# Optimization experiments

Hardware: AMD Instinct MI355X
Metric: run time of the kernel (lower is better)

Reference implementation:

```python
import jax, jax.numpy as jnp
import numpy as np

B, S, DM, TD, H, HD = 2, 2048, 1024, 1024, 16, 64


def setup_inputs() -> dict:
    key = jax.random.key(0)
    k1, k2, k3, k4 = jax.random.split(key, 4)
    query = jax.random.normal(k1, (B, S, DM), dtype=jnp.float32)
    # fused QKV projection weight (nn.Linear weight layout: [out, in]) and output proj
    W_in = jax.random.normal(k2, (3 * TD, DM), dtype=jnp.float32) * 0.02
    W_out = jax.random.normal(k3, (DM, TD), dtype=jnp.float32) * 0.02
    # standard RoPE tables, broadcastable against [B, H, S, HD]
    inv_freq = 1.0 / (10000.0 ** (jnp.arange(0, HD, 2, dtype=jnp.float32) / HD))
    t = jnp.arange(S, dtype=jnp.float32)
    freqs = jnp.outer(t, inv_freq)                      # [S, HD/2]
    emb = jnp.concatenate([freqs, freqs], axis=-1)      # [S, HD]
    sin_q = jnp.sin(emb)[None, None]                    # [1,1,S,HD]
    cos_q = jnp.cos(emb)[None, None]
    # padding mask over keys: first length[b] positions valid (>= S/2 so no NaN rows)
    lengths = jax.random.randint(k4, (B,), S // 2, S + 1)
    attn_mask = jnp.arange(S)[None, :] < lengths[:, None]  # [B, S] bool
    return {"query": query, "W_in": W_in, "W_out": W_out,
            "sin_q": sin_q, "cos_q": cos_q, "attn_mask": attn_mask}


def _rotate_half(x):
    x1, x2 = jnp.split(x, 2, axis=-1)
    return jnp.concatenate([-x2, x1], axis=-1)


def reference(query, W_in, W_out, sin_q, cos_q, attn_mask):
    # fused QKV projection (proj_in, bias=False)
    qkv = query @ W_in.T                                # [B, S, 3*TD]
    q, k, v = jnp.split(qkv, 3, axis=-1)
    to_heads = lambda x: x.reshape(B, S, H, HD).transpose(0, 2, 1, 3)  # [B,H,S,HD]
    q, k, v = to_heads(q), to_heads(k), to_heads(v)
    # RoPE (prefix = 0 since sin covers full sequence)
    q = q * cos_q + _rotate_half(q) * sin_q
    k = k * cos_q + _rotate_half(k) * sin_q
    # SDPA with padding-mask bias + causal mask
    scale = 1.0 / jnp.sqrt(jnp.float32(HD))
    scores = jnp.einsum('bhqd,bhkd->bhqk', q, k) * scale  # [B,H,S,S]
    causal = jnp.arange(S)[:, None] >= jnp.arange(S)[None, :]  # [S, S]
    mask = attn_mask[:, None, None, :] & causal[None, None]    # [B,1,S,S]
    scores = jnp.where(mask, scores, -jnp.inf)
    attn = jax.nn.softmax(scores, axis=-1)
    out = jnp.einsum('bhqk,bhkd->bhqd', attn, v)        # [B,H,S,HD]
    out = out.transpose(0, 2, 1, 3).reshape(B, S, TD)
    return out @ W_out.T                                 # [B, S, DM]
```

## Files before the change

### kernel.cpp

```cpp
#include <hip/hip_runtime.h>
#include <hip/hip_bf16.h>

#define B_ 2
#define S_ 2048
#define DM_ 1024
#define TD_ 1024
#define H_ 16
#define HD_ 64

using bf16 = __hip_bfloat16;
typedef __attribute__((ext_vector_type(8))) short s8v;
typedef __attribute__((ext_vector_type(4))) float f4v;

__device__ __forceinline__ f4v mfma_bf16(s8v a, s8v b, f4v c) {
    return __builtin_amdgcn_mfma_f32_16x16x32_bf16(a, b, c, 0, 0, 0);
}

__device__ __forceinline__ unsigned cvt_pk_bf16(float a, float b) {
    unsigned r;
    asm("v_cvt_pk_bf16_f32 %0, %1, %2" : "=v"(r) : "v"(a), "v"(b));
    return r;
}
__device__ __forceinline__ int2 pack4bf(float a, float b, float c, float d) {
    int2 r;
    r.x = (int)cvt_pk_bf16(a, b);
    r.y = (int)cvt_pk_bf16(c, d);
    return r;
}

__device__ __forceinline__ bool detect_f32(const unsigned int* __restrict__ cosw) {
    return (cosw[0] & 0xFFFFu) == 0u;
}

__device__ __forceinline__ float ld_f(const void* p, int idx, bool f32) {
    return f32 ? ((const float*)p)[idx]
               : __bfloat162float(((const bf16*)p)[idx]);
}

__device__ __forceinline__ void gload_lds16(const bf16* g, void* l) {
    __builtin_amdgcn_global_load_lds(
        (const __attribute__((address_space(1))) unsigned int*)(const void*)g,
        (__attribute__((address_space(3))) unsigned int*)l,
        16, 0, 0);
}

#define NQ_  (B_ * S_ * DM_)
#define NWI_ (3 * TD_ * DM_)
#define NWO_ (DM_ * TD_)
#define NCVT_BLOCKS ((NQ_ + NWI_ + NWO_) / 2048)

__global__ __launch_bounds__(256)
void prep_all(const void* __restrict__ q, const void* __restrict__ wi,
              const void* __restrict__ wo, bf16* __restrict__ dst,
              const void* __restrict__ mask, int* __restrict__ lengths,
              const unsigned int* __restrict__ cosw) {
    const int bid = blockIdx.x;
    if (bid < NCVT_BLOCKS) {
        const bool f32 = detect_f32(cosw);
        int i = (bid * 256 + threadIdx.x) * 8;
        const void* src; int off;
        if (i < NQ_)              { src = q;  off = i; }
        else if (i < NQ_ + NWI_)  { src = wi; off = i - NQ_; }
        else                      { src = wo; off = i - NQ_ - NWI_; }
        if (f32) {
            const float* p = (const float*)src + off;
            float4 x = *reinterpret_cast<const float4*>(p);
            float4 y = *reinterpret_cast<const float4*>(p + 4);
            union { unsigned u[4]; int4 v; } t;
            t.u[0] = cvt_pk_bf16(x.x, x.y);
            t.u[1] = cvt_pk_bf16(x.z, x.w);
            t.u[2] = cvt_pk_bf16(y.x, y.y);
            t.u[3] = cvt_pk_bf16(y.z, y.w);
            *reinterpret_cast<int4*>(dst + i) = t.v;
        } else {
            *reinterpret_cast<int4*>(dst + i) =
                *reinterpret_cast<const int4*>((const bf16*)src + off);
        }
        return;
    }
    int b = bid - NCVT_BLOCKS;
    unsigned int w0 = ((const unsigned int*)mask)[0];
    int enc;
    if (w0 == 1u) enc = 0;
    else if (w0 == 0x01010101u) enc = 1;
    else if (w0 == 0x3F803F80u) enc = 2;
    else enc = 3;
    int cnt = 0;
    for (int s = threadIdx.x; s < S_; s += 256) {
        int i = b * S_ + s;
        bool v;
        if (enc == 0)      v = ((const int*)mask)[i] != 0;
        else if (enc == 1) v = ((const unsigned char*)mask)[i] != 0;
        else if (enc == 2) v = ((const unsigned short*)mask)[i] != 0;
        else               v = ((const float*)mask)[i] != 0.f;
        cnt += v ? 1 : 0;
    }
    __shared__ int red[256];
    red[threadIdx.x] = cnt;
    __syncthreads();
    for (int off = 128; off > 0; off >>= 1) {
        if (threadIdx.x < off) red[threadIdx.x] += red[threadIdx.x + off];
        __syncthreads();
    }
    if (threadIdx.x == 0) lengths[b] = red[0];
}

__global__ __launch_bounds__(256)
void gemm_nt(const bf16* __restrict__ A, const bf16* __restrict__ Bm,
             void* __restrict__ C, int M, int N, int K,
             int c_dyn, const unsigned int* __restrict__ cosw) {
    __shared__ bf16 lds_a[128 * 64];
    __shared__ bf16 lds_b[128 * 64];

    const bool cf32 = c_dyn && detect_f32(cosw);

    const int t = threadIdx.x;
    const int wave = t >> 6, lane = t & 63;
    const int quad = lane >> 4, l16 = lane & 15;
    const int wm = wave >> 1, wn = wave & 1;
    const int m0 = blockIdx.y * 128, n0 = blockIdx.x * 128;
    const int wuni = __builtin_amdgcn_readfirstlane(wave);

    f4v acc[4][4];
    #pragma unroll
    for (int i = 0; i < 4; i++)
        #pragma unroll
        for (int j = 0; j < 4; j++)
            acc[i][j] = f4v{0.f, 0.f, 0.f, 0.f};

    for (int k0 = 0; k0 < K; k0 += 64) {
        __syncthreads();
        #pragma unroll
        for (int i = 0; i < 4; i++) {
            int ci = i * 256 + t;
            int row = ci >> 3;
            int csrc = (ci & 7) ^ (row & 7);
            gload_lds16(A + (size_t)(m0 + row) * K + k0 + csrc * 8,
                        (char*)lds_a + i * 4096 + wuni * 1024);
            gload_lds16(Bm + (size_t)(n0 + row) * K + k0 + csrc * 8,
                        (char*)lds_b + i * 4096 + wuni * 1024);
        }
        __syncthreads();

        #pragma unroll
        for (int kk = 0; kk < 2; kk++) {
            s8v afr[4], bfr[4];
            #pragma unroll
            for (int mb = 0; mb < 4; mb++) {
                int r = wm * 64 + mb * 16 + l16;
                int ch = (kk * 4 + quad) ^ (l16 & 7);
                afr[mb] = *reinterpret_cast<const s8v*>(&lds_a[r * 64 + ch * 8]);
            }
            #pragma unroll
            for (int nb = 0; nb < 4; nb++) {
                int r = wn * 64 + nb * 16 + l16;
                int ch = (kk * 4 + quad) ^ (l16 & 7);
                bfr[nb] = *reinterpret_cast<const s8v*>(&lds_b[r * 64 + ch * 8]);
            }
            #pragma unroll
            for (int mb = 0; mb < 4; mb++)
                #pragma unroll
                for (int nb = 0; nb < 4; nb++)
                    acc[mb][nb] = mfma_bf16(bfr[nb], afr[mb], acc[mb][nb]);
        }
    }

    #pragma unroll
    for (int mb = 0; mb < 4; mb++) {
        int m = m0 + wm * 64 + mb * 16 + l16;
        #pragma unroll
        for (int nb = 0; nb < 4; nb++) {
            int n = n0 + wn * 64 + nb * 16 + quad * 4;
            f4v v = acc[mb][nb];
            if (cf32) {
                *reinterpret_cast<f4v*>(&((float*)C)[(size_t)m * N + n]) = v;
            } else {
                *reinterpret_cast<int2*>(&((bf16*)C)[(size_t)m * N + n]) =
                    pack4bf(v[0], v[1], v[2], v[3]);
            }
        }
    }
}

__global__ __launch_bounds__(256)
void rope_vt(const bf16* __restrict__ qkv,
             const void* __restrict__ sin_t, const void* __restrict__ cos_t,
             bf16* __restrict__ Qh, bf16* __restrict__ Kt, bf16* __restrict__ Vt) {
    __shared__ bf16 tile[64 * 72];
    const int bid = blockIdx.x;
    if (bid < 16384) {
        const bool f32 = detect_f32((const unsigned int*)cos_t);
        int idx = bid * 256 + threadIdx.x;
        int d = idx & 63;
        int h = (idx >> 6) & 15;
        int s = (idx >> 10) & 2047;
        int b = idx >> 21;
        size_t row = (size_t)(b * S_ + s) * 3072;
        int col  = h * 64 + d;
        int colp = h * 64 + ((d + 32) & 63);
        float sgn = (d < 32) ? -1.f : 1.f;
        float cs = ld_f(cos_t, s * 64 + d, f32);
        float sn = ld_f(sin_t, s * 64 + d, f32);
        float q  = __bfloat162float(qkv[row + col]);
        float qp = __bfloat162float(qkv[row + colp]);
        float k  = __bfloat162float(qkv[row + 1024 + col]);
        float kp = __bfloat162float(qkv[row + 1024 + colp]);
        Qh[((size_t)((b * H_ + h) * S_ + s)) * 64 + d] =
            __float2bfloat16((q * cs + sgn * qp * sn) * 0.180336880f);
        size_t ktile = ((size_t)(b * H_ + h) * 32 + (s >> 6)) * 4096;
        int dp = ((((d >> 3) ^ (s & 7)) << 3) | (d & 7));
        Kt[ktile + (s & 63) * 64 + dp] = __float2bfloat16(k * cs + sgn * kp * sn);
        return;
    }
    const int vid = bid - 16384;
    const int sb = vid & 31, h = (vid >> 5) & 15, b = vid >> 9;
    const int t = threadIdx.x;
    #pragma unroll
    for (int i = 0; i < 2; i++) {
        int id = i * 256 + t;
        int row = id >> 3, c = id & 7;
        *reinterpret_cast<int4*>(&tile[row * 72 + c * 8]) =
            *reinterpret_cast<const int4*>(
                qkv + (size_t)(b * S_ + sb * 64 + row) * 3072 + 2048 + h * 64 + c * 8);
    }
    __syncthreads();
    const size_t tb = ((size_t)(b * H_ + h) * 32 + sb) * 4096;
    #pragma unroll
    for (int i = 0; i < 2; i++) {
        int id = i * 256 + t;
        int d = id >> 3, kc = id & 7;
        union { short s[8]; int4 v; } u;
        #pragma unroll
        for (int e = 0; e < 8; e++)
            u.s[e] = reinterpret_cast<const short*>(tile)[(kc * 8 + e) * 72 + d];
        *reinterpret_cast<int4*>(Vt + tb + d * 64 + ((kc ^ (d & 7)) * 8)) = u.v;
    }
}

__global__ __launch_bounds__(512)
void attn_fused(const bf16* __restrict__ Qh, const bf16* __restrict__ Kt,
                const bf16* __restrict__ Vt, const int* __restrict__ lengths,
                bf16* __restrict__ out) {
    __shared__ bf16 k_buf[2 * 4096];
    __shared__ bf16 v_buf[2 * 4096];
    __shared__ bf16 lds_p[8 * 16 * 72];

    const int t = threadIdx.x, wave = t >> 6, lane = t & 63;
    const int quad = lane >> 4, l16 = lane & 15;
    const int grp = wave >> 2;
    const int wq = wave & 3;

    const int bid = blockIdx.x;
    const int xcd = bid & 7;
    int g, bh;
    if (bid < 256) {
        int r = bid >> 3;
        bh = xcd * 4 + (r & 3);
        g = r >> 2;
    } else {
        int r = (bid - 256) >> 3;
        bh = xcd * 4 + (r & 3);
        g = 15 - (r >> 2);
    }
    const int qb = 2 * g + grp;
    const int b = bh >> 4, h = bh & 15;

    const size_t hb = (size_t)bh * S_ * 64;
    const bf16* Ktp = Kt + (size_t)bh * 32 * 4096;
    const bf16* Vtp = Vt + (size_t)bh * 32 * 4096;
    const int wuni = __builtin_amdgcn_readfirstlane(wave);
    int len_raw = lengths[b];
    const int len_b = len_raw < 1 ? 1 : (len_raw > S_ ? S_ : len_raw);
    const int nkt_len = (len_b + 63) >> 6;

    const int nkt_w = (qb + 1) < nkt_len ? (qb + 1) : nkt_len;
    const int nkt   = (2 * g + 2) < nkt_len ? (2 * g + 2) : nkt_len;

    const int qrow_g = qb * 64 + wq * 16 + l16;
    const int kmax = (qrow_g < len_b - 1) ? qrow_g : (len_b - 1);

    s8v qf[2];
    {
        const bf16* qptr = Qh + hb + (size_t)qrow_g * 64 + quad * 8;
        qf[0] = *reinterpret_cast<const s8v*>(qptr);
        qf[1] = *reinterpret_cast<const s8v*>(qptr + 32);
    }

    f4v o_acc[4];
    #pragma unroll
    for (int a = 0; a < 4; a++) o_acc[a] = f4v{0.f, 0.f, 0.f, 0.f};
    float l_sum = 0.f;

    auto stageK = [&](int x) {
        gload_lds16(Ktp + (size_t)x * 4096 + t * 8,
                    (char*)k_buf + (x & 1) * 8192 + wuni * 1024);
    };
    auto stageV = [&](int x) {
        gload_lds16(Vtp + (size_t)x * 4096 + t * 8,
                    (char*)v_buf + (x & 1) * 8192 + wuni * 1024);
    };

    f4v s_prev[4];
    auto process_tile = [&](int pt) {
        const bf16* vb = v_buf + (pt & 1) * 4096;
        const int pbase = pt * 64;
        const bool tail = (pt == qb) || (pbase + 64 > len_b);
        #pragma unroll
        for (int a = 0; a < 4; a++) {
            float e0[4];
            #pragma unroll
            for (int r = 0; r < 4; r++) {
                float e = __builtin_amdgcn_exp2f(s_prev[a][r]);
                if (tail) {
                    int key = pbase + a * 16 + quad * 4 + r;
                    e = (key <= kmax) ? e : 0.f;
                }
                e0[r] = e;
                l_sum += e;
            }
            *reinterpret_cast<int2*>(
                &lds_p[(wave * 16 + l16) * 72 + a * 16 + quad * 4]) =
                pack4bf(e0[0], e0[1], e0[2], e0[3]);
        }
        asm volatile("s_waitcnt lgkmcnt(0)" ::: "memory");
        #pragma unroll
        for (int kk = 0; kk < 2; kk++) {
            s8v pf = *reinterpret_cast<const s8v*>(
                &lds_p[(wave * 16 + l16) * 72 + kk * 32 + quad * 8]);
            #pragma unroll
            for (int a = 0; a < 4; a++) {
                int ch = (kk * 4 + quad) ^ (l16 & 7);
                s8v vf = *reinterpret_cast<const s8v*>(
                    &vb[(a * 16 + l16) * 64 + ch * 8]);
                o_acc[a] = mfma_bf16(vf, pf, o_acc[a]);
            }
        }
    };

    stageK(0);
    __syncthreads();

    for (int kt = 0; kt < nkt; kt++) {
        stageV(kt);
        if (kt + 1 < nkt) stageK(kt + 1);

        const bool act = (kt < nkt_w);
        f4v sn[4];
        if (act) {
            const bf16* kb = k_buf + (kt & 1) * 4096;
            #pragma unroll
            for (int a = 0; a < 4; a++) sn[a] = f4v{0.f, 0.f, 0.f, 0.f};
            #pragma unroll
            for (int kk = 0; kk < 2; kk++) {
                #pragma unroll
                for (int a = 0; a < 4; a++) {
                    int ch = (kk * 4 + quad) ^ (l16 & 7);
                    s8v kf = *reinterpret_cast<const s8v*>(
                        &kb[(a * 16 + l16) * 64 + ch * 8]);
                    sn[a] = mfma_bf16(kf, qf[kk], sn[a]);
                }
            }
        }

        if (kt >= 1 && (kt - 1) < nkt_w) process_tile(kt - 1);

        if (act) {
            #pragma unroll
            for (int a = 0; a < 4; a++) s_prev[a] = sn[a];
        }

        __syncthreads();
    }
    if (nkt_w == nkt) process_tile(nkt_w - 1);

    l_sum += __shfl_xor(l_sum, 16);
    l_sum += __shfl_xor(l_sum, 32);
    float inv_l = 1.f / l_sum;
    size_t orow = ((size_t)(b * S_ + qrow_g)) * TD_ + h * 64;
    #pragma unroll
    for (int a = 0; a < 4; a++) {
        *reinterpret_cast<int2*>(&out[orow + a * 16 + quad * 4]) =
            pack4bf(o_acc[a][0] * inv_l, o_acc[a][1] * inv_l,
                    o_acc[a][2] * inv_l, o_acc[a][3] * inv_l);
    }
}

extern "C" void kernel_launch(void* const* d_in, const int* in_sizes, int n_in,
                              void* d_out, int out_size, void* d_ws, size_t ws_size,
                              hipStream_t stream) {
    const void* query = d_in[0];
    const void* W_in  = d_in[1];
    const void* W_out = d_in[2];
    const void* sin_q = d_in[3];
    const void* cos_q = d_in[4];
    const void* mask  = d_in[5];
    const unsigned int* cosw = (const unsigned int*)cos_q;

    const size_t nQ  = NQ_;
    const size_t nWi = NWI_;
    const size_t nWo = NWO_;

    bf16* qkv  = (bf16*)d_ws;
    bf16* Qh   = qkv + (size_t)4096 * 3072;
    bf16* Kt   = Qh + nQ;
    bf16* qbf  = Kt + nQ;
    bf16* wibf = qbf + nQ;
    bf16* wobf = wibf + nWi;
    int* lengths = (int*)(wobf + nWo);
    bf16* Vt   = qbf;
    bf16* attn = qkv;

    prep_all<<<NCVT_BLOCKS + B_, 256, 0, stream>>>(
        query, W_in, W_out, qbf, mask, lengths, cosw);

    dim3 g1(3072 / 128, 4096 / 128);
    gemm_nt<<<g1, 256, 0, stream>>>(qbf, wibf, qkv, 4096, 3072, 1024, 0, cosw);

    rope_vt<<<16384 + 1024, 256, 0, stream>>>(qkv, sin_q, cos_q, Qh, Kt, Vt);

    attn_fused<<<512, 512, 0, stream>>>(Qh, Kt, Vt, lengths, attn);

    dim3 g2(1024 / 128, 4096 / 128);
    gemm_nt<<<g2, 256, 0, stream>>>(attn, wobf, d_out, 4096, 1024, 1024, 1, cosw);
}
```

Measured before the change: 197.5 us.

## Fuse RoPE and Q/K head layout into QKV GEMM epilogue

The QKV projection GEMM now applies RoPE, the Q scaling, and the swizzled K tile layout directly in its epilogue, using the fact that each wave's 64 columns cover one head so rotate-half pairs sit in registers (nb and nb^2). V is written to a compact temporary and transposed by a smaller dedicated kernel. This removes the full qkv write and re-read plus the elementwise RoPE kernel, at the cost of a heavier GEMM epilogue with scattered 8-byte stores.

Measured after the change: 208.6 us. 1.06x slower.

```diff
diff --git a/kernel.cpp b/kernel.cpp
--- a/kernel.cpp
+++ b/kernel.cpp
@@ -32,9 +32,15 @@
     return (cosw[0] & 0xFFFFu) == 0u;
 }
 
-__device__ __forceinline__ float ld_f(const void* p, int idx, bool f32) {
-    return f32 ? ((const float*)p)[idx]
-               : __bfloat162float(((const bf16*)p)[idx]);
+__device__ __forceinline__ void ld4_f(const void* p, int idx, bool f32, float* o) {
+    if (f32) {
+        float4 v = *reinterpret_cast<const float4*>((const float*)p + idx);
+        o[0] = v.x; o[1] = v.y; o[2] = v.z; o[3] = v.w;
+    } else {
+        const bf16* q = (const bf16*)p + idx;
+        #pragma unroll
+        for (int i = 0; i < 4; i++) o[i] = __bfloat162float(q[i]);
+    }
 }
 
 __device__ __forceinline__ void gload_lds16(const bf16* g, void* l) {
@@ -107,12 +113,12 @@
 
 __global__ __launch_bounds__(256)
 void gemm_nt(const bf16* __restrict__ A, const bf16* __restrict__ Bm,
-             void* __restrict__ C, int M, int N, int K,
-             int c_dyn, const unsigned int* __restrict__ cosw) {
+             void* __restrict__ C, int M, int N, int K, int mode,
+             const void* __restrict__ sin_t, const void* __restrict__ cos_t,
+             bf16* __restrict__ Qh, bf16* __restrict__ Kt,
+             bf16* __restrict__ Vtmp, const unsigned int* __restrict__ cosw) {
     __shared__ bf16 lds_a[128 * 64];
     __shared__ bf16 lds_b[128 * 64];
-
-    const bool cf32 = c_dyn && detect_f32(cosw);
 
     const int t = threadIdx.x;
     const int wave = t >> 6, lane = t & 63;
@@ -165,6 +171,56 @@
         }
     }
 
+    if (mode == 2) {
+        const bool f32 = detect_f32(cosw);
+        const int nc = n0 + wn * 64;
+        const int region = nc >> 10;
+        const int h = (nc >> 6) & 15;
+        #pragma unroll
+        for (int mb = 0; mb < 4; mb++) {
+            int m = m0 + wm * 64 + mb * 16 + l16;
+            int s = m & (S_ - 1), bb = m >> 11;
+            if (region == 2) {
+                #pragma unroll
+                for (int nb = 0; nb < 4; nb++) {
+                    int vcol = (nc - 2048) + nb * 16 + quad * 4;
+                    f4v v = acc[mb][nb];
+                    *reinterpret_cast<int2*>(&Vtmp[(size_t)m * 1024 + vcol]) =
+                        pack4bf(v[0], v[1], v[2], v[3]);
+                }
+            } else {
+                #pragma unroll
+                for (int nb = 0; nb < 4; nb++) {
+                    int d0 = nb * 16 + quad * 4;
+                    float cs[4], sn[4];
+                    ld4_f(cos_t, s * 64 + d0, f32, cs);
+                    ld4_f(sin_t, s * 64 + d0, f32, sn);
+                    float sgn = (nb < 2) ? -1.f : 1.f;
+                    float ov[4];
+                    #pragma unroll
+                    for (int rr = 0; rr < 4; rr++)
+                        ov[rr] = acc[mb][nb][rr] * cs[rr] +
+                                 sgn * acc[mb][nb ^ 2][rr] * sn[rr];
+                    if (region == 0) {
+                        #pragma unroll
+                        for (int rr = 0; rr < 4; rr++) ov[rr] *= 0.180336880f;
+                        size_t o = (((size_t)(bb * 16 + h)) * S_ + s) * 64 + d0;
+                        *reinterpret_cast<int2*>(&Qh[o]) =
+                            pack4bf(ov[0], ov[1], ov[2], ov[3]);
+                    } else {
+                        size_t ktile = ((size_t)(bb * 16 + h) * 32 + (s >> 6)) * 4096;
+                        int chunk = (d0 >> 3) ^ (s & 7);
+                        size_t o = ktile + (s & 63) * 64 + chunk * 8 + (d0 & 7);
+                        *reinterpret_cast<int2*>(&Kt[o]) =
+                            pack4bf(ov[0], ov[1], ov[2], ov[3]);
+                    }
+                }
+            }
+        }
+        return;
+    }
+
+    const bool cf32 = (mode == 1) && detect_f32(cosw);
     #pragma unroll
     for (int mb = 0; mb < 4; mb++) {
         int m = m0 + wm * 64 + mb * 16 + l16;
@@ -183,36 +239,9 @@
 }
 
 __global__ __launch_bounds__(256)
-void rope_vt(const bf16* __restrict__ qkv,
-             const void* __restrict__ sin_t, const void* __restrict__ cos_t,
-             bf16* __restrict__ Qh, bf16* __restrict__ Kt, bf16* __restrict__ Vt) {
+void v_transpose(const bf16* __restrict__ Vtmp, bf16* __restrict__ Vt) {
     __shared__ bf16 tile[64 * 72];
-    const int bid = blockIdx.x;
-    if (bid < 16384) {
-        const bool f32 = detect_f32((const unsigned int*)cos_t);
-        int idx = bid * 256 + threadIdx.x;
-        int d = idx & 63;
-        int h = (idx >> 6) & 15;
-        int s = (idx >> 10) & 2047;
-        int b = idx >> 21;
-        size_t row = (size_t)(b * S_ + s) * 3072;
-        int col  = h * 64 + d;
-        int colp = h * 64 + ((d + 32) & 63);
-        float sgn = (d < 32) ? -1.f : 1.f;
-        float cs = ld_f(cos_t, s * 64 + d, f32);
-        float sn = ld_f(sin_t, s * 64 + d, f32);
-        float q  = __bfloat162float(qkv[row + col]);
-        float qp = __bfloat162float(qkv[row + colp]);
-        float k  = __bfloat162float(qkv[row + 1024 + col]);
-        float kp = __bfloat162float(qkv[row + 1024 + colp]);
-        Qh[((size_t)((b * H_ + h) * S_ + s)) * 64 + d] =
-            __float2bfloat16((q * cs + sgn * qp * sn) * 0.180336880f);
-        size_t ktile = ((size_t)(b * H_ + h) * 32 + (s >> 6)) * 4096;
-        int dp = ((((d >> 3) ^ (s & 7)) << 3) | (d & 7));
-        Kt[ktile + (s & 63) * 64 + dp] = __float2bfloat16(k * cs + sgn * kp * sn);
-        return;
-    }
-    const int vid = bid - 16384;
+    const int vid = blockIdx.x;
     const int sb = vid & 31, h = (vid >> 5) & 15, b = vid >> 9;
     const int t = threadIdx.x;
     #pragma unroll
@@ -221,7 +250,7 @@
         int row = id >> 3, c = id & 7;
         *reinterpret_cast<int4*>(&tile[row * 72 + c * 8]) =
             *reinterpret_cast<const int4*>(
-                qkv + (size_t)(b * S_ + sb * 64 + row) * 3072 + 2048 + h * 64 + c * 8);
+                Vtmp + (size_t)(b * S_ + sb * 64 + row) * 1024 + h * 64 + c * 8);
     }
     __syncthreads();
     const size_t tb = ((size_t)(b * H_ + h) * 32 + sb) * 4096;
@@ -400,26 +429,28 @@
     const size_t nWi = NWI_;
     const size_t nWo = NWO_;
 
-    bf16* qkv  = (bf16*)d_ws;
-    bf16* Qh   = qkv + (size_t)4096 * 3072;
+    bf16* Vtmp = (bf16*)d_ws;
+    bf16* Qh   = Vtmp + nQ;
     bf16* Kt   = Qh + nQ;
     bf16* qbf  = Kt + nQ;
     bf16* wibf = qbf + nQ;
     bf16* wobf = wibf + nWi;
     int* lengths = (int*)(wobf + nWo);
     bf16* Vt   = qbf;
-    bf16* attn = qkv;
+    bf16* attn = Vtmp;
 
     prep_all<<<NCVT_BLOCKS + B_, 256, 0, stream>>>(
         query, W_in, W_out, qbf, mask, lengths, cosw);
 
     dim3 g1(3072 / 128, 4096 / 128);
-    gemm_nt<<<g1, 256, 0, stream>>>(qbf, wibf, qkv, 4096, 3072, 1024, 0, cosw);
-
-    rope_vt<<<16384 + 1024, 256, 0, stream>>>(qkv, sin_q, cos_q, Qh, Kt, Vt);
+    gemm_nt<<<g1, 256, 0, stream>>>(qbf, wibf, nullptr, 4096, 3072, 1024, 2,
+                                    sin_q, cos_q, Qh, Kt, Vtmp, cosw);
+
+    v_transpose<<<1024, 256, 0, stream>>>(Vtmp, Vt);
 
     attn_fused<<<512, 512, 0, stream>>>(Qh, Kt, Vt, lengths, attn);
 
     dim3 g2(1024 / 128, 4096 / 128);
-    gemm_nt<<<g2, 256, 0, stream>>>(attn, wobf, d_out, 4096, 1024, 1024, 1, cosw);
-}
+    gemm_nt<<<g2, 256, 0, stream>>>(attn, wobf, d_out, 4096, 1024, 1024, 1,
+                                    nullptr, nullptr, nullptr, nullptr, nullptr, cosw);
+}
```
